# Optimization experiments

Hardware: AMD Instinct MI355X
Metric: run time of the kernel (lower is better)

## Reference

```python
import jax, jax.numpy as jnp
import numpy as np

H = 450    # hidden_size (JTNN default)
LAT = 56   # latent_size (tree_vec dim)
V = 780    # vocab size
T = 1024   # n_trees
L = 24     # nodes per tree (path topology)


def _tree_meta(Ln):
    # forward edge i: (i, i+1) eid=i ; reverse edge i: (i+1, i) eid=(Ln-1)+i
    n_f = Ln - 1
    eids, preds, srcs, dsts, labels = [], [], [], [], []
    for i in range(n_f):  # forward DFS steps
        eids.append(i); srcs.append(i); dsts.append(i + 1)
        preds.append(i - 1 if i > 0 else -1); labels.append(0)
    for k in range(n_f):  # backtrack DFS steps (reverse edges, deepest first)
        i = n_f - 1 - k
        eids.append(n_f + i); srcs.append(i + 1); dsts.append(i)
        preds.append(n_f + i + 1 if i < n_f - 1 else -1); labels.append(1)
    # incoming edges of the dst node v (for the node 'pull' h = sum of m)
    in1 = [d - 1 if d > 0 else -1 for d in dsts]
    in2 = [n_f + d if d < n_f else -1 for d in dsts]
    meta = [np.asarray(a, np.int32) for a in (eids, preds, srcs, dsts, in1, in2)]
    return meta, np.asarray(labels, np.float32)


def setup_inputs():
    key = jax.random.key(0)
    ks = jax.random.split(key, 12)
    s = 0.05
    return {
        "wid": jax.random.randint(ks[0], (T, L), 0, V, dtype=jnp.int32),
        "tree_vec": jax.random.normal(ks[1], (T, LAT), jnp.float32),
        "emb": jax.random.normal(ks[2], (V, H)) * s,
        "W_w": jax.random.normal(ks[3], (H + LAT, H)) * s, "W_b": jnp.zeros((H,)),
        "U_w": jax.random.normal(ks[4], (2 * H + LAT, H)) * s, "U_b": jnp.zeros((H,)),
        "Wo_w": jax.random.normal(ks[5], (H, V)) * s, "Wo_b": jnp.zeros((V,)),
        "Us_w": jax.random.normal(ks[6], (H, 1)) * s, "Us_b": jnp.zeros((1,)),
        "Wz_w": jax.random.normal(ks[7], (2 * H, H)) * s, "Wz_b": jnp.zeros((H,)),
        "Wr_w": jax.random.normal(ks[8], (H, H)) * s,
        "Ur_w": jax.random.normal(ks[9], (H, H)) * s, "Ur_b": jnp.zeros((H,)),
        "Wh_w": jax.random.normal(ks[10], (2 * H, H)) * s, "Wh_b": jnp.zeros((H,)),
    }


def reference(wid, tree_vec, emb, W_w, W_b, U_w, U_b, Wo_w, Wo_b, Us_w, Us_b,
              Wz_w, Wz_b, Wr_w, Ur_w, Ur_b, Wh_w, Wh_b):
    Tn, Ln = wid.shape
    n_f = Ln - 1
    nE = 2 * n_f
    meta, labels = _tree_meta(Ln)
    xs = tuple(jnp.asarray(a) for a in meta)
    x = emb[wid]                                  # [T, L, H] node features
    m0 = jnp.zeros((Tn, nE, H), x.dtype)
    rm0 = jnp.zeros((Tn, nE, H), x.dtype)

    def step(carry, sx_):
        m, rm = carry
        eid, pred, src, dst, i1, i2 = sx_
        gp = jnp.maximum(pred, 0)
        s = jnp.where(pred >= 0, m[:, gp], 0.0)        # line-graph pull: sum of m
        arm = jnp.where(pred >= 0, rm[:, gp], 0.0)     # accum_rm
        sxn = x[:, src]                                # src_x
        dxn = x[:, dst]                                # dst_x
        z = jax.nn.sigmoid(jnp.concatenate([sxn, s], 1) @ Wz_w + Wz_b)
        mt = jnp.tanh(jnp.concatenate([sxn, arm], 1) @ Wh_w + Wh_b)
        m_new = (1.0 - z) * s + z * mt
        r = jax.nn.sigmoid(dxn @ Wr_w + m_new @ Ur_w + Ur_b)
        m = m.at[:, eid].set(m_new)
        rm = rm.at[:, eid].set(r * m_new)
        # node pull on v: h_v = sum of m over incoming edges (post edge update)
        h_v = (jnp.where(i1 >= 0, m[:, jnp.maximum(i1, 0)], 0.0)
               + jnp.where(i2 >= 0, m[:, jnp.maximum(i2, 0)], 0.0))
        return (m, rm), (h_v, dxn)

    (_, _), (hs, xvs) = jax.lax.scan(step, (m0, rm0), xs)  # [nE, T, H] each

    tv_steps = jnp.broadcast_to(tree_vec, (nE, Tn, LAT))
    p_in = jnp.concatenate([
        jnp.concatenate([x[:, 0], jnp.zeros((Tn, H), x.dtype), tree_vec], 1),
        jnp.concatenate([xvs, hs, tv_steps], -1).reshape(-1, 2 * H + LAT),
    ], 0)
    q_in = jnp.concatenate([
        jnp.concatenate([jnp.zeros((Tn, H), x.dtype), tree_vec], 1),
        jnp.concatenate([hs[:n_f], tv_steps[:n_f]], -1).reshape(-1, H + LAT),
    ], 0)
    p_targets = jnp.concatenate([jnp.repeat(jnp.asarray(1.0 - labels), Tn),
                                 jnp.zeros((Tn,), jnp.float32)])
    q_targets = wid.T.reshape(-1)

    q_logits = jax.nn.relu(q_in @ W_w + W_b) @ Wo_w + Wo_b
    p_logit = (jax.nn.relu(p_in @ U_w + U_b) @ Us_w + Us_b)[:, 0]
    p_loss = jnp.sum(p_targets * jax.nn.softplus(-p_logit)
                     + (1.0 - p_targets) * jax.nn.softplus(p_logit)) / Tn
    logp = jax.nn.log_softmax(q_logits, -1)
    q_loss = -jnp.sum(jnp.take_along_axis(logp, q_targets[:, None], 1)) / Tn
    p_acc = jnp.mean(((p_logit > 0).astype(jnp.int32) == p_targets.astype(jnp.int32)).astype(jnp.float32))
    q_acc = jnp.mean((jnp.argmax(q_logits, 1) == q_targets).astype(jnp.float32))
    return (q_loss, p_loss, q_acc, p_acc)
```

## Files before the change

kernel.cpp:

```cpp
#include <hip/hip_runtime.h>
#include <hip/hip_bf16.h>
#include <math.h>

#define H 450
#define HP 464
#define KP 480
#define LAT 56
#define V 780
#define LW 24
#define NE 46
#define NF 23
#define SLOT (1024*HP)
#define SROWS 2048
#define QROWS (24*1024)
#define PROWS (47*1024)
#define PTGT  (23*1024)
#define QBLK 6144

typedef __hip_bfloat16 bf16;
typedef __attribute__((ext_vector_type(8))) short short8;
typedef __attribute__((ext_vector_type(4))) float f32x4;

#define MFMA16(a,b,c) __builtin_amdgcn_mfma_f32_16x16x32_bf16(a,b,c,0,0,0)

__device__ __forceinline__ float sigm(float x) { return 1.f / (1.f + expf(-x)); }
__device__ __forceinline__ float toF(bf16 x) { return __bfloat162float(x); }
__device__ __forceinline__ void stV(float* p, float v) { *p = v; }
__device__ __forceinline__ void stV(bf16* p, float v) { *p = __float2bfloat16(v); }
__device__ __forceinline__ short8 ld8(const bf16* p) { return *reinterpret_cast<const short8*>(p); }

__device__ __forceinline__ void gl_lds(const bf16* g, bf16* l) {
    __builtin_amdgcn_global_load_lds(
        (const __attribute__((address_space(1))) void*)g,
        (__attribute__((address_space(3))) void*)l, 16, 0, 0);
}

__device__ __forceinline__ void xcd_decode(int b, int C, int& row0, int& col0) {
    int rres = b & 7;
    int colt = (b >> 3) % C;
    int g    = b / (8 * C);
    row0 = (rres + 8 * g) * 64;
    col0 = colt * 64;
}
__device__ __forceinline__ void xcd_decode128(int b, int C, int& row0, int& col0) {
    int rres = b & 7;
    int colt = (b >> 3) % C;
    int g    = b / (8 * C);
    row0 = (rres + 8 * g) * 128;
    col0 = colt * 128;
}

__global__ __launch_bounds__(256)
void make_bt(const float* __restrict__ src, int K, int N, int ld,
             bf16* __restrict__ dst, int npad) {
    int idx = blockIdx.x * 256 + threadIdx.x;
    if (idx >= npad * KP) return;
    int n = idx / KP, k = idx - n * KP;
    float v = (n < N && k < K) ? src[(size_t)k * ld + n] : 0.f;
    dst[idx] = __float2bfloat16(v);
}

__global__ __launch_bounds__(256)
void zero_init(float* __restrict__ out, float* __restrict__ Sb, int n) {
    int i = blockIdx.x * 256 + threadIdx.x;
    if (i < 4) out[i] = 0.f;
    if (i < n) Sb[i] = 0.f;
}

__global__ __launch_bounds__(256)
void gather_x(const float* __restrict__ emb, const int* __restrict__ wid,
              bf16* __restrict__ x_all) {
    int e = blockIdx.x * 256 + threadIdx.x;
    if (e >= 24 * 1024 * 225) return;
    int row = e / 225, h2 = e - row * 225;
    int t = row >> 10, n = row & 1023;
    int v = wid[n * LW + t];
    float2 x = ((const float2*)(emb + (size_t)v * H))[h2];
    bf16* dst = x_all + (size_t)row * HP + 2 * h2;
    dst[0] = __float2bfloat16(x.x);
    dst[1] = __float2bfloat16(x.y);
}

template<typename TC>
__global__ __launch_bounds__(256)
void gemm128(const bf16* __restrict__ A, int lda,
             const bf16* __restrict__ Bt, int N, int cblk,
             TC* __restrict__ C, int ldc,
             const float* __restrict__ bias,
             const float* __restrict__ addrow, int addld, int relu) {
    __shared__ bf16 As[128 * 32];
    __shared__ bf16 Bs[128 * 32];
    int tid = threadIdx.x;
    int lane = tid & 63, wave = tid >> 6;
    int wx = wave & 1, wy = wave >> 1;
    int lrow = lane & 15, quad = lane >> 4;
    int row0, col0;
    xcd_decode128(blockIdx.x, cblk, row0, col0);
    f32x4 acc[4][4] = {};
    for (int k0i = 0; k0i < 15; k0i++) {
        int k0 = k0i * 32;
#pragma unroll
        for (int r = 0; r < 2; r++) {
            int t = r * 256 + tid;
            int row = t >> 2, ko = (t & 3) * 8;
            gl_lds(A  + (size_t)(row0 + row) * lda + k0 + ko, As + t * 8);
            gl_lds(Bt + (size_t)(col0 + row) * KP  + k0 + ko, Bs + t * 8);
        }
        __syncthreads();
        short8 a[4], b[4];
#pragma unroll
        for (int f = 0; f < 4; f++)
            a[f] = ld8(As + (wy * 64 + f * 16 + lrow) * 32 + quad * 8);
#pragma unroll
        for (int f = 0; f < 4; f++)
            b[f] = ld8(Bs + (wx * 64 + f * 16 + lrow) * 32 + quad * 8);
#pragma unroll
        for (int fi = 0; fi < 4; fi++)
#pragma unroll
            for (int fj = 0; fj < 4; fj++)
                acc[fi][fj] = MFMA16(a[fi], b[fj], acc[fi][fj]);
        __syncthreads();
    }
#pragma unroll
    for (int fi = 0; fi < 4; fi++)
#pragma unroll
        for (int e = 0; e < 4; e++) {
            int r = row0 + wy * 64 + fi * 16 + quad * 4 + e;
#pragma unroll
            for (int fj = 0; fj < 4; fj++) {
                int c = col0 + wx * 64 + fj * 16 + lrow;
                if (c >= N) continue;
                float v = acc[fi][fj][e];
                if (bias) v += bias[c];
                if (addrow) v += addrow[(size_t)(r & 1023) * addld + c];
                if (relu) v = fmaxf(v, 0.f);
                stV(&C[(size_t)r * ldc + c], v);
            }
        }
}

__global__ __launch_bounds__(256)
void p_gemm128(const bf16* __restrict__ hs, const bf16* __restrict__ UbT,
               const bf16* __restrict__ XUa, const float* __restrict__ Ptv,
               const float* __restrict__ Us, float* __restrict__ pl) {
    __shared__ bf16 As[128 * 32];
    __shared__ bf16 Bs[128 * 32];
    int tid = threadIdx.x;
    int lane = tid & 63, wave = tid >> 6;
    int wx = wave & 1, wy = wave >> 1;
    int lrow = lane & 15, quad = lane >> 4;
    int row0, col0;
    xcd_decode128(blockIdx.x, 4, row0, col0);
    f32x4 acc[4][4] = {};
    for (int k0i = 0; k0i < 15; k0i++) {
        int k0 = k0i * 32;
#pragma unroll
        for (int r = 0; r < 2; r++) {
            int t = r * 256 + tid;
            int row = t >> 2, ko = (t & 3) * 8;
            gl_lds(hs  + (size_t)(row0 + row) * HP + k0 + ko, As + t * 8);
            gl_lds(UbT + (size_t)(col0 + row) * KP + k0 + ko, Bs + t * 8);
        }
        __syncthreads();
        short8 a[4], b[4];
#pragma unroll
        for (int f = 0; f < 4; f++)
            a[f] = ld8(As + (wy * 64 + f * 16 + lrow) * 32 + quad * 8);
#pragma unroll
        for (int f = 0; f < 4; f++)
            b[f] = ld8(Bs + (wx * 64 + f * 16 + lrow) * 32 + quad * 8);
#pragma unroll
        for (int fi = 0; fi < 4; fi++)
#pragma unroll
            for (int fj = 0; fj < 4; fj++)
                acc[fi][fj] = MFMA16(a[fi], b[fj], acc[fi][fj]);
        __syncthreads();
    }
    int t0 = row0 >> 10;
#pragma unroll
    for (int fi = 0; fi < 4; fi++)
#pragma unroll
        for (int e = 0; e < 4; e++) {
            int r = row0 + wy * 64 + fi * 16 + quad * 4 + e;
            int t = r >> 10, n = r & 1023;
            int dst = (t < 23) ? (t + 1) : (45 - t);
            float part = 0.f;
#pragma unroll
            for (int fj = 0; fj < 4; fj++) {
                int c = col0 + wx * 64 + fj * 16 + lrow;
                if (c < H) {
                    float h = fmaxf(acc[fi][fj][e] + toF(XUa[((size_t)dst * 1024 + n) * H + c])
                                    + Ptv[(size_t)n * H + c], 0.f);
                    part += h * Us[c];
                }
            }
#pragma unroll
            for (int off = 1; off < 16; off <<= 1)
                part += __shfl_xor(part, off);
            if (lrow == 0) atomicAdd(&pl[1024 + r], part);
        }
    (void)t0;
}

__global__ __launch_bounds__(256)
void tv_gemm(const float* __restrict__ tv, const float* __restrict__ Wlat,
             const float* __restrict__ bias, float* __restrict__ out) {
    int n = blockIdx.y;
    int c = blockIdx.x * 256 + threadIdx.x;
    __shared__ float tvs[LAT];
    if (threadIdx.x < LAT) tvs[threadIdx.x] = tv[n * LAT + threadIdx.x];
    __syncthreads();
    if (c < H) {
        float a = bias[c];
#pragma unroll 8
        for (int k = 0; k < LAT; k++) a += tvs[k] * Wlat[(size_t)k * H + c];
        out[(size_t)n * H + c] = a;
    }
}

__global__ __launch_bounds__(256)
void scan_k1(const bf16* __restrict__ AsF, const bf16* __restrict__ AsB,
             const bf16* __restrict__ Arm,
             const bf16* __restrict__ BzT, const bf16* __restrict__ BhT,
             const bf16* __restrict__ Xz, const bf16* __restrict__ Xh,
             float* __restrict__ Sb, bf16* __restrict__ hsF, bf16* __restrict__ hsB,
             int u, int skip) {
    int tid = threadIdx.x;
    int lane = tid & 63, wave = tid >> 6;
    int wx = wave & 1, wy = wave >> 1;
    int lrow = lane & 15, quad = lane >> 4;
    int row0, col0;
    xcd_decode(blockIdx.x, 8, row0, col0);
    bool fwd = row0 < 1024;
    int rb = row0 & 1023;
    f32x4 az[2][2] = {}, ah[2][2] = {};
    if (!skip) {
        const bf16* As = (fwd ? AsF : AsB) + (size_t)(rb + wy * 32 + lrow) * HP + quad * 8;
        const bf16* Ar = Arm + (size_t)(row0 + wy * 32 + lrow) * HP + quad * 8;
        const bf16* bz0 = BzT + (size_t)(col0 + wx * 32 + lrow) * KP + quad * 8;
        const bf16* bh0 = BhT + (size_t)(col0 + wx * 32 + lrow) * KP + quad * 8;
        for (int k = 0; k < 15; k++) {
            short8 s0 = ld8(As + k * 32);
            short8 s1 = ld8(As + (size_t)16 * HP + k * 32);
            short8 r0 = ld8(Ar + k * 32);
            short8 r1 = ld8(Ar + (size_t)16 * HP + k * 32);
            short8 z0 = ld8(bz0 + k * 32);
            short8 z1 = ld8(bz0 + 16 * KP + k * 32);
            short8 h0 = ld8(bh0 + k * 32);
            short8 h1 = ld8(bh0 + 16 * KP + k * 32);
            az[0][0] = MFMA16(s0, z0, az[0][0]);
            az[0][1] = MFMA16(s0, z1, az[0][1]);
            az[1][0] = MFMA16(s1, z0, az[1][0]);
            az[1][1] = MFMA16(s1, z1, az[1][1]);
            ah[0][0] = MFMA16(r0, h0, ah[0][0]);
            ah[0][1] = MFMA16(r0, h1, ah[0][1]);
            ah[1][0] = MFMA16(r1, h0, ah[1][0]);
            ah[1][1] = MFMA16(r1, h1, ah[1][1]);
        }
    }
    int src = fwd ? u : 23 - u;
    bf16* hso = fwd ? hsF : hsB;
#pragma unroll
    for (int i = 0; i < 2; i++)
#pragma unroll
        for (int e = 0; e < 4; e++) {
            int r = row0 + wy * 32 + i * 16 + quad * 4 + e;
            int n = r & 1023;
#pragma unroll
            for (int j = 0; j < 2; j++) {
                int c = col0 + wx * 32 + j * 16 + lrow;
                if (c >= H) continue;
                float zp = az[i][j][e] + toF(Xz[((size_t)src * 1024 + n) * H + c]);
                float hp = ah[i][j][e] + toF(Xh[((size_t)src * 1024 + n) * H + c]);
                float s  = Sb[(size_t)r * H + c];
                float z  = sigm(zp);
                float mt = tanhf(hp);
                float mn = (1.f - z) * s + z * mt;
                Sb[(size_t)r * H + c] = mn;
                hso[(size_t)n * HP + c] = __float2bfloat16(mn);
            }
        }
}

__global__ __launch_bounds__(256)
void scan_k2(const bf16* __restrict__ AmF, const bf16* __restrict__ AmB,
             const bf16* __restrict__ UrT, const bf16* __restrict__ Xr,
             const float* __restrict__ Sb, bf16* __restrict__ RMb, int u) {
    int tid = threadIdx.x;
    int lane = tid & 63, wave = tid >> 6;
    int wx = wave & 1, wy = wave >> 1;
    int lrow = lane & 15, quad = lane >> 4;
    int row0, col0;
    xcd_decode(blockIdx.x, 8, row0, col0);
    bool fwd = row0 < 1024;
    int rb = row0 & 1023;
    const bf16* Am = (fwd ? AmF : AmB) + (size_t)(rb + wy * 32 + lrow) * HP + quad * 8;
    const bf16* b0 = UrT + (size_t)(col0 + wx * 32 + lrow) * KP + quad * 8;
    f32x4 acc[2][2] = {};
    for (int k = 0; k < 15; k++) {
        short8 a0 = ld8(Am + k * 32);
        short8 a1 = ld8(Am + (size_t)16 * HP + k * 32);
        short8 w0 = ld8(b0 + k * 32);
        short8 w1 = ld8(b0 + 16 * KP + k * 32);
        acc[0][0] = MFMA16(a0, w0, acc[0][0]);
        acc[0][1] = MFMA16(a0, w1, acc[0][1]);
        acc[1][0] = MFMA16(a1, w0, acc[1][0]);
        acc[1][1] = MFMA16(a1, w1, acc[1][1]);
    }
    int dst = fwd ? (u + 1) : (22 - u);
#pragma unroll
    for (int i = 0; i < 2; i++)
#pragma unroll
        for (int e = 0; e < 4; e++) {
            int r = row0 + wy * 32 + i * 16 + quad * 4 + e;
            int n = r & 1023;
#pragma unroll
            for (int j = 0; j < 2; j++) {
                int c = col0 + wx * 32 + j * 16 + lrow;
                if (c >= H) continue;
                float rp = acc[i][j][e] + toF(Xr[((size_t)dst * 1024 + n) * H + c]);
                float rr = sigm(rp);
                RMb[(size_t)r * HP + c] = __float2bfloat16(rr * Sb[(size_t)r * H + c]);
            }
        }
}

__global__ __launch_bounds__(256)
void hv_fixup(bf16* __restrict__ hs) {
    int idx = blockIdx.x * 256 + threadIdx.x;
    if (idx >= 22 * SLOT) return;
    int tl = idx / SLOT;
    int rem = idx - tl * SLOT;
    size_t a = (size_t)(23 + tl) * SLOT + rem;
    size_t b = (size_t)(21 - tl) * SLOT + rem;
    hs[a] = __float2bfloat16(toF(hs[a]) + toF(hs[b]));
}

__global__ __launch_bounds__(256)
void q_root(const float* __restrict__ Qtv, bf16* __restrict__ qh) {
    int idx = blockIdx.x * 256 + threadIdx.x;
    if (idx >= 1024 * H) return;
    int n = idx / H, c = idx - n * H;
    qh[(size_t)n * HP + c] = __float2bfloat16(fmaxf(Qtv[idx], 0.f));
}

__global__ __launch_bounds__(256)
void q_reduce(const float* __restrict__ ql, const int* __restrict__ wid,
              float* __restrict__ qred) {
    int wave = threadIdx.x >> 6, lane = threadIdx.x & 63;
    int r = blockIdx.x * 4 + wave;
    int t = r >> 10, n = r & 1023;
    int tgt = wid[n * LW + t];
    const float4* row4 = (const float4*)(ql + (size_t)r * V);
    float m = -3.4e38f, s = 0.f; int mi = 0x7fffffff;
#pragma unroll
    for (int k = 0; k < 4; k++) {
        int c4 = lane + 64 * k;
        if (c4 < 195) {
            float4 v4 = row4[c4];
            float vv[4] = {v4.x, v4.y, v4.z, v4.w};
#pragma unroll
            for (int e = 0; e < 4; e++) {
                float v = vv[e];
                if (v > m) { s = s * __expf(m - v) + 1.f; m = v; mi = c4 * 4 + e; }
                else s += __expf(v - m);
            }
        }
    }
#pragma unroll
    for (int off = 1; off < 64; off <<= 1) {
        float m2 = __shfl_xor(m, off);
        float s2 = __shfl_xor(s, off);
        int   i2 = __shfl_xor(mi, off);
        if (m2 > m || (m2 == m && i2 < mi)) {
            s = s2 + s * __expf(m - m2);
            m = m2; mi = i2;
        } else {
            s = s + s2 * __expf(m2 - m);
        }
    }
    __shared__ float lred[4][2];
    if (lane == 0) {
        float lse = m + logf(s);
        lred[wave][0] = lse - ql[(size_t)r * V + tgt];
        lred[wave][1] = (mi == tgt) ? 1.f : 0.f;
    }
    __syncthreads();
    if (threadIdx.x == 0) {
        qred[blockIdx.x * 2]     = lred[0][0] + lred[1][0] + lred[2][0] + lred[3][0];
        qred[blockIdx.x * 2 + 1] = lred[0][1] + lred[1][1] + lred[2][1] + lred[3][1];
    }
}

__global__ __launch_bounds__(256)
void q_final(const float* __restrict__ qred, float* __restrict__ out) {
    int tid = threadIdx.x;
    float L = 0.f, A = 0.f;
    for (int i = tid; i < QBLK; i += 256) { L += qred[2 * i]; A += qred[2 * i + 1]; }
    __shared__ float s1[256], s2[256];
    s1[tid] = L; s2[tid] = A;
    __syncthreads();
    for (int k = 128; k > 0; k >>= 1) {
        if (tid < k) { s1[tid] += s1[tid + k]; s2[tid] += s2[tid + k]; }
        __syncthreads();
    }
    if (tid == 0) {
        out[0] = s1[0] * (1.f / 1024.f);
        out[2] = s2[0] * (1.f / 24576.f);
    }
}

__global__ __launch_bounds__(256)
void p_init(float* __restrict__ pl, const float* __restrict__ Us_b) {
    int idx = blockIdx.x * 256 + threadIdx.x;
    if (idx < PROWS) pl[idx] = Us_b[0];
}

__global__ __launch_bounds__(256)
void p_root(const bf16* __restrict__ XUa, const float* __restrict__ Ptv,
            const float* __restrict__ Us, float* __restrict__ pl) {
    int n = blockIdx.x;
    int tid = threadIdx.x;
    const bf16* xa = XUa + (size_t)n * H;
    const float* pt = Ptv + (size_t)n * H;
    float s = 0.f;
    for (int c = tid; c < H; c += 256)
        s += fmaxf(toF(xa[c]) + pt[c], 0.f) * Us[c];
    __shared__ float red[256];
    red[tid] = s;
    __syncthreads();
    for (int k = 128; k > 0; k >>= 1) {
        if (tid < k) red[tid] += red[tid + k];
        __syncthreads();
    }
    if (tid == 0) atomicAdd(&pl[n], red[0]);
}

__global__ __launch_bounds__(256)
void p_final(const float* __restrict__ pl, float* __restrict__ out) {
    int r = blockIdx.x * 256 + threadIdx.x;
    int tid = threadIdx.x;
    float loss = 0.f, acc = 0.f;
    if (r < PROWS) {
        float l = pl[r];
        int tgt = (r < PTGT) ? 1 : 0;
        float x = tgt ? -l : l;
        loss = fmaxf(x, 0.f) + log1pf(expf(-fabsf(x)));
        int pred = (l > 0.f) ? 1 : 0;
        acc = (pred == tgt) ? 1.f : 0.f;
    }
    __shared__ float s1[256], s2[256];
    s1[tid] = loss; s2[tid] = acc;
    __syncthreads();
    for (int k = 128; k > 0; k >>= 1) {
        if (tid < k) { s1[tid] += s1[tid + k]; s2[tid] += s2[tid + k]; }
        __syncthreads();
    }
    if (tid == 0) {
        atomicAdd(&out[1], s1[0] * (1.f / 1024.f));
        atomicAdd(&out[3], s2[0] * (1.f / 48128.f));
    }
}

extern "C" void kernel_launch(void* const* d_in, const int* in_sizes, int n_in,
                              void* d_out, int out_size, void* d_ws, size_t ws_size,
                              hipStream_t stream) {
    const int*   wid  = (const int*)  d_in[0];
    const float* tv   = (const float*)d_in[1];
    const float* emb  = (const float*)d_in[2];
    const float* W_w  = (const float*)d_in[3];
    const float* W_b  = (const float*)d_in[4];
    const float* U_w  = (const float*)d_in[5];
    const float* U_b  = (const float*)d_in[6];
    const float* Wo_w = (const float*)d_in[7];
    const float* Wo_b = (const float*)d_in[8];
    const float* Us_w = (const float*)d_in[9];
    const float* Us_b = (const float*)d_in[10];
    const float* Wz_w = (const float*)d_in[11];
    const float* Wz_b = (const float*)d_in[12];
    const float* Wr_w = (const float*)d_in[13];
    const float* Ur_w = (const float*)d_in[14];
    const float* Ur_b = (const float*)d_in[15];
    const float* Wh_w = (const float*)d_in[16];
    const float* Wh_b = (const float*)d_in[17];
    float* out = (float*)d_out;

    char* base = (char*)d_ws;
    const size_t XBb = (size_t)QROWS * H * 2;
    bf16*  Xz   = (bf16*)(base);
    bf16*  Xh   = (bf16*)(base + XBb);
    bf16*  Xr   = (bf16*)(base + 2 * XBb);
    bf16*  XUa  = (bf16*)(base + 3 * XBb);
    bf16*  hs   = (bf16*)(base + 4 * XBb);
    bf16*  x_all = hs;
    char*  p1   = base + 4 * XBb + (size_t)NE * SLOT * 2;
    bf16*  RMb  = (bf16*)p1;                p1 += (size_t)SROWS * HP * 2;
    float* Sb   = (float*)p1;               p1 += (size_t)SROWS * H * 4;
    float* Qtv  = (float*)p1;               p1 += (size_t)1024 * H * 4;
    float* Ptv  = (float*)p1;               p1 += (size_t)1024 * H * 4;
    float* pl   = (float*)p1;               p1 += (size_t)PROWS * 4;
    float* qred = (float*)p1;               p1 += (size_t)QBLK * 2 * 4;
    bf16*  BT   = (bf16*)p1;
    const size_t BTS = (size_t)512 * KP;
    bf16 *WztT = BT,           *WhtT = BT + BTS,     *WrT = BT + 2*BTS,
         *UaT  = BT + 3*BTS,   *WzbT = BT + 4*BTS,   *WhbT = BT + 5*BTS,
         *UrT  = BT + 6*BTS,   *UbT  = BT + 7*BTS,   *WtopT = BT + 8*BTS,
         *WoT  = BT + 9*BTS;
    bf16*  qh = (bf16*)base;
    float* ql = (float*)(base + (size_t)QROWS * HP * 2);

    zero_init<<<(SROWS * H + 255) / 256, 256, 0, stream>>>(out, Sb, SROWS * H);
    int btg = (512 * KP + 255) / 256;
    make_bt<<<btg, 256, 0, stream>>>(Wz_w,            H, H, H, WztT, 512);
    make_bt<<<btg, 256, 0, stream>>>(Wh_w,            H, H, H, WhtT, 512);
    make_bt<<<btg, 256, 0, stream>>>(Wr_w,            H, H, H, WrT,  512);
    make_bt<<<btg, 256, 0, stream>>>(U_w,             H, H, H, UaT,  512);
    make_bt<<<btg, 256, 0, stream>>>(Wz_w + 450*450,  H, H, H, WzbT, 512);
    make_bt<<<btg, 256, 0, stream>>>(Wh_w + 450*450,  H, H, H, WhbT, 512);
    make_bt<<<btg, 256, 0, stream>>>(Ur_w,            H, H, H, UrT,  512);
    make_bt<<<btg, 256, 0, stream>>>(U_w + 450*450,   H, H, H, UbT,  512);
    make_bt<<<btg, 256, 0, stream>>>(W_w,             H, H, H, WtopT, 512);
    make_bt<<<(896 * KP + 255) / 256, 256, 0, stream>>>(Wo_w, H, V, V, WoT, 896);

    gather_x<<<(24 * 1024 * 225 + 255) / 256, 256, 0, stream>>>(emb, wid, x_all);
    int gPre = (QROWS / 128) * 4;
    gemm128<bf16><<<gPre, 256, 0, stream>>>(x_all, HP, WztT, H, 4, Xz,  H, Wz_b, (const float*)nullptr, H, 0);
    gemm128<bf16><<<gPre, 256, 0, stream>>>(x_all, HP, WhtT, H, 4, Xh,  H, Wh_b, (const float*)nullptr, H, 0);
    gemm128<bf16><<<gPre, 256, 0, stream>>>(x_all, HP, WrT,  H, 4, Xr,  H, Ur_b, (const float*)nullptr, H, 0);
    gemm128<bf16><<<gPre, 256, 0, stream>>>(x_all, HP, UaT,  H, 4, XUa, H, (const float*)nullptr, (const float*)nullptr, H, 0);

    tv_gemm<<<dim3(2, 1024), 256, 0, stream>>>(tv, W_w + 450*450, W_b, Qtv);
    tv_gemm<<<dim3(2, 1024), 256, 0, stream>>>(tv, U_w + 900*450, U_b, Ptv);

    for (int u = 0; u < 23; u++) {
        const bf16* AsF = hs + (size_t)(u - 1) * SLOT;
        const bf16* AsB = hs + (size_t)(22 + u) * SLOT;
        scan_k1<<<256, 256, 0, stream>>>(AsF, AsB, RMb, WzbT, WhbT, Xz, Xh,
                                         Sb, hs + (size_t)u * SLOT,
                                         hs + (size_t)(23 + u) * SLOT, u, u == 0 ? 1 : 0);
        if (u < 22)
            scan_k2<<<256, 256, 0, stream>>>(hs + (size_t)u * SLOT, hs + (size_t)(23 + u) * SLOT,
                                             UrT, Xr, Sb, RMb, u);
    }
    hv_fixup<<<(22 * SLOT + 255) / 256, 256, 0, stream>>>(hs);

    p_init<<<(PROWS + 255) / 256, 256, 0, stream>>>(pl, Us_b);
    p_root<<<1024, 256, 0, stream>>>(XUa, Ptv, Us_w, pl);
    p_gemm128<<<(PROWS - 1024) / 128 * 4, 256, 0, stream>>>(hs, UbT, XUa, Ptv, Us_w, pl);
    p_final<<<PROWS / 256, 256, 0, stream>>>(pl, out);

    q_root<<<(1024 * H + 255) / 256, 256, 0, stream>>>(Qtv, qh);
    gemm128<bf16><<<(NF * 1024 / 128) * 4, 256, 0, stream>>>(hs, HP, WtopT, H, 4,
                                                             qh + (size_t)1024 * HP, HP,
                                                             (const float*)nullptr, Qtv, H, 1);
    gemm128<float><<<(QROWS / 128) * 7, 256, 0, stream>>>(qh, HP, WoT, V, 7, ql, V,
                                                          Wo_b, (const float*)nullptr, H, 0);
    q_reduce<<<QBLK, 256, 0, stream>>>(ql, wid, qred);
    q_final<<<1, 256, 0, stream>>>(qred, out);

    (void)in_sizes; (void)n_in; (void)out_size; (void)ws_size;
}
```

Before: 1.197 ms.

## Fuse four input-projection GEMMs into one wide GEMM and swizzle LDS tiles

The four x_all projections (Wz, Wh, Wr/Ur bias, U top) become a single GEMM over a concatenated 1800-column weight matrix with a packed bias vector. The epilogue splits columns into the Xz/Xh/Xr/XUa buffers, which sit next to each other in the workspace. This cuts the column padding waste from 512 to 450 per matrix and reads the A tiles in one pass instead of four launches. Separately, all 128x128 GEMMs apply an XOR-style rotation to the k-chunk offset in LDS to reduce bank conflicts on the fragment reads.

Result: faster. 1.104 ms (-7.8%).

```diff
diff --git a/kernel.cpp b/kernel.cpp
--- a/kernel.cpp
+++ b/kernel.cpp
@@ -16,6 +16,7 @@
 #define PROWS (47*1024)
 #define PTGT  (23*1024)
 #define QBLK 6144
+#define XBSZ ((size_t)QROWS * H)
 
 typedef __hip_bfloat16 bf16;
 typedef __attribute__((ext_vector_type(8))) short short8;
@@ -58,6 +59,18 @@
     int n = idx / KP, k = idx - n * KP;
     float v = (n < N && k < K) ? src[(size_t)k * ld + n] : 0.f;
     dst[idx] = __float2bfloat16(v);
+}
+
+__global__ __launch_bounds__(256)
+void pack_bias(const float* __restrict__ zb, const float* __restrict__ hb,
+               const float* __restrict__ rb, float* __restrict__ bias4) {
+    int i = blockIdx.x * 256 + threadIdx.x;
+    if (i >= 1856) return;
+    float v = 0.f;
+    if (i < 450)       v = zb[i];
+    else if (i < 900)  v = hb[i - 450];
+    else if (i < 1350) v = rb[i - 900];
+    bias4[i] = v;
 }
 
 __global__ __launch_bounds__(256)
@@ -94,6 +107,7 @@
     int lane = tid & 63, wave = tid >> 6;
     int wx = wave & 1, wy = wave >> 1;
     int lrow = lane & 15, quad = lane >> 4;
+    int perm = ((quad + (lrow >> 1)) & 3) * 8;
     int row0, col0;
     xcd_decode128(blockIdx.x, cblk, row0, col0);
     f32x4 acc[4][4] = {};
@@ -101,19 +115,20 @@
         int k0 = k0i * 32;
 #pragma unroll
         for (int r = 0; r < 2; r++) {
-            int t = r * 256 + tid;
-            int row = t >> 2, ko = (t & 3) * 8;
-            gl_lds(A  + (size_t)(row0 + row) * lda + k0 + ko, As + t * 8);
-            gl_lds(Bt + (size_t)(col0 + row) * KP  + k0 + ko, Bs + t * 8);
+            int tt = r * 256 + tid;
+            int row = tt >> 2, cl = tt & 3;
+            int cg = (cl - (row >> 1)) & 3;
+            gl_lds(A  + (size_t)(row0 + row) * lda + k0 + cg * 8, As + tt * 8);
+            gl_lds(Bt + (size_t)(col0 + row) * KP  + k0 + cg * 8, Bs + tt * 8);
         }
         __syncthreads();
         short8 a[4], b[4];
 #pragma unroll
         for (int f = 0; f < 4; f++)
-            a[f] = ld8(As + (wy * 64 + f * 16 + lrow) * 32 + quad * 8);
+            a[f] = ld8(As + (wy * 64 + f * 16 + lrow) * 32 + perm);
 #pragma unroll
         for (int f = 0; f < 4; f++)
-            b[f] = ld8(Bs + (wx * 64 + f * 16 + lrow) * 32 + quad * 8);
+            b[f] = ld8(Bs + (wx * 64 + f * 16 + lrow) * 32 + perm);
 #pragma unroll
         for (int fi = 0; fi < 4; fi++)
 #pragma unroll
@@ -140,6 +155,63 @@
 }
 
 __global__ __launch_bounds__(256)
+void gemm128_pre(const bf16* __restrict__ A,
+                 const bf16* __restrict__ Bt,
+                 bf16* __restrict__ X0,
+                 const float* __restrict__ bias4) {
+    __shared__ bf16 As[128 * 32];
+    __shared__ bf16 Bs[128 * 32];
+    int tid = threadIdx.x;
+    int lane = tid & 63, wave = tid >> 6;
+    int wx = wave & 1, wy = wave >> 1;
+    int lrow = lane & 15, quad = lane >> 4;
+    int perm = ((quad + (lrow >> 1)) & 3) * 8;
+    int row0, col0;
+    xcd_decode128(blockIdx.x, 15, row0, col0);
+    f32x4 acc[4][4] = {};
+    for (int k0i = 0; k0i < 15; k0i++) {
+        int k0 = k0i * 32;
+#pragma unroll
+        for (int r = 0; r < 2; r++) {
+            int tt = r * 256 + tid;
+            int row = tt >> 2, cl = tt & 3;
+            int cg = (cl - (row >> 1)) & 3;
+            gl_lds(A  + (size_t)(row0 + row) * HP + k0 + cg * 8, As + tt * 8);
+            gl_lds(Bt + (size_t)(col0 + row) * KP + k0 + cg * 8, Bs + tt * 8);
+        }
+        __syncthreads();
+        short8 a[4], b[4];
+#pragma unroll
+        for (int f = 0; f < 4; f++)
+            a[f] = ld8(As + (wy * 64 + f * 16 + lrow) * 32 + perm);
+#pragma unroll
+        for (int f = 0; f < 4; f++)
+            b[f] = ld8(Bs + (wx * 64 + f * 16 + lrow) * 32 + perm);
+#pragma unroll
+        for (int fi = 0; fi < 4; fi++)
+#pragma unroll
+            for (int fj = 0; fj < 4; fj++)
+                acc[fi][fj] = MFMA16(a[fi], b[fj], acc[fi][fj]);
+        __syncthreads();
+    }
+#pragma unroll
+    for (int fi = 0; fi < 4; fi++)
+#pragma unroll
+        for (int e = 0; e < 4; e++) {
+            int r = row0 + wy * 64 + fi * 16 + quad * 4 + e;
+#pragma unroll
+            for (int fj = 0; fj < 4; fj++) {
+                int c = col0 + wx * 64 + fj * 16 + lrow;
+                if (c >= 1800) continue;
+                int mm = c / 450;
+                int cc = c - mm * 450;
+                float v = acc[fi][fj][e] + bias4[c];
+                X0[(size_t)mm * XBSZ + (size_t)r * H + cc] = __float2bfloat16(v);
+            }
+        }
+}
+
+__global__ __launch_bounds__(256)
 void p_gemm128(const bf16* __restrict__ hs, const bf16* __restrict__ UbT,
                const bf16* __restrict__ XUa, const float* __restrict__ Ptv,
                const float* __restrict__ Us, float* __restrict__ pl) {
@@ -149,6 +221,7 @@
     int lane = tid & 63, wave = tid >> 6;
     int wx = wave & 1, wy = wave >> 1;
     int lrow = lane & 15, quad = lane >> 4;
+    int perm = ((quad + (lrow >> 1)) & 3) * 8;
     int row0, col0;
     xcd_decode128(blockIdx.x, 4, row0, col0);
     f32x4 acc[4][4] = {};
@@ -156,19 +229,20 @@
         int k0 = k0i * 32;
 #pragma unroll
         for (int r = 0; r < 2; r++) {
-            int t = r * 256 + tid;
-            int row = t >> 2, ko = (t & 3) * 8;
-            gl_lds(hs  + (size_t)(row0 + row) * HP + k0 + ko, As + t * 8);
-            gl_lds(UbT + (size_t)(col0 + row) * KP + k0 + ko, Bs + t * 8);
+            int tt = r * 256 + tid;
+            int row = tt >> 2, cl = tt & 3;
+            int cg = (cl - (row >> 1)) & 3;
+            gl_lds(hs  + (size_t)(row0 + row) * HP + k0 + cg * 8, As + tt * 8);
+            gl_lds(UbT + (size_t)(col0 + row) * KP + k0 + cg * 8, Bs + tt * 8);
         }
         __syncthreads();
         short8 a[4], b[4];
 #pragma unroll
         for (int f = 0; f < 4; f++)
-            a[f] = ld8(As + (wy * 64 + f * 16 + lrow) * 32 + quad * 8);
+            a[f] = ld8(As + (wy * 64 + f * 16 + lrow) * 32 + perm);
 #pragma unroll
         for (int f = 0; f < 4; f++)
-            b[f] = ld8(Bs + (wx * 64 + f * 16 + lrow) * 32 + quad * 8);
+            b[f] = ld8(Bs + (wx * 64 + f * 16 + lrow) * 32 + perm);
 #pragma unroll
         for (int fi = 0; fi < 4; fi++)
 #pragma unroll
@@ -176,7 +250,6 @@
                 acc[fi][fj] = MFMA16(a[fi], b[fj], acc[fi][fj]);
         __syncthreads();
     }
-    int t0 = row0 >> 10;
 #pragma unroll
     for (int fi = 0; fi < 4; fi++)
 #pragma unroll
@@ -199,7 +272,6 @@
                 part += __shfl_xor(part, off);
             if (lrow == 0) atomicAdd(&pl[1024 + r], part);
         }
-    (void)t0;
 }
 
 __global__ __launch_bounds__(256)
@@ -486,7 +558,7 @@
     float* out = (float*)d_out;
 
     char* base = (char*)d_ws;
-    const size_t XBb = (size_t)QROWS * H * 2;
+    const size_t XBb = XBSZ * 2;
     bf16*  Xz   = (bf16*)(base);
     bf16*  Xh   = (bf16*)(base + XBb);
     bf16*  Xr   = (bf16*)(base + 2 * XBb);
@@ -500,21 +572,26 @@
     float* Ptv  = (float*)p1;               p1 += (size_t)1024 * H * 4;
     float* pl   = (float*)p1;               p1 += (size_t)PROWS * 4;
     float* qred = (float*)p1;               p1 += (size_t)QBLK * 2 * 4;
+    float* bias4 = (float*)p1;              p1 += (size_t)1856 * 4;
     bf16*  BT   = (bf16*)p1;
-    const size_t BTS = (size_t)512 * KP;
-    bf16 *WztT = BT,           *WhtT = BT + BTS,     *WrT = BT + 2*BTS,
-         *UaT  = BT + 3*BTS,   *WzbT = BT + 4*BTS,   *WhbT = BT + 5*BTS,
-         *UrT  = BT + 6*BTS,   *UbT  = BT + 7*BTS,   *WtopT = BT + 8*BTS,
-         *WoT  = BT + 9*BTS;
+    bf16* BT4   = BT;
+    bf16* WzbT  = BT + (size_t)1856 * KP;
+    bf16* WhbT  = WzbT + (size_t)512 * KP;
+    bf16* UrT   = WhbT + (size_t)512 * KP;
+    bf16* UbT   = UrT  + (size_t)512 * KP;
+    bf16* WtopT = UbT  + (size_t)512 * KP;
+    bf16* WoT   = WtopT + (size_t)512 * KP;
     bf16*  qh = (bf16*)base;
     float* ql = (float*)(base + (size_t)QROWS * HP * 2);
 
     zero_init<<<(SROWS * H + 255) / 256, 256, 0, stream>>>(out, Sb, SROWS * H);
     int btg = (512 * KP + 255) / 256;
-    make_bt<<<btg, 256, 0, stream>>>(Wz_w,            H, H, H, WztT, 512);
-    make_bt<<<btg, 256, 0, stream>>>(Wh_w,            H, H, H, WhtT, 512);
-    make_bt<<<btg, 256, 0, stream>>>(Wr_w,            H, H, H, WrT,  512);
-    make_bt<<<btg, 256, 0, stream>>>(U_w,             H, H, H, UaT,  512);
+    int btg450 = (450 * KP + 255) / 256;
+    make_bt<<<btg450, 256, 0, stream>>>(Wz_w, H, H, H, BT4,                        450);
+    make_bt<<<btg450, 256, 0, stream>>>(Wh_w, H, H, H, BT4 + (size_t)450 * KP,     450);
+    make_bt<<<btg450, 256, 0, stream>>>(Wr_w, H, H, H, BT4 + (size_t)900 * KP,     450);
+    make_bt<<<(506 * KP + 255) / 256, 256, 0, stream>>>(U_w, H, H, H, BT4 + (size_t)1350 * KP, 506);
+    pack_bias<<<8, 256, 0, stream>>>(Wz_b, Wh_b, Ur_b, bias4);
     make_bt<<<btg, 256, 0, stream>>>(Wz_w + 450*450,  H, H, H, WzbT, 512);
     make_bt<<<btg, 256, 0, stream>>>(Wh_w + 450*450,  H, H, H, WhbT, 512);
     make_bt<<<btg, 256, 0, stream>>>(Ur_w,            H, H, H, UrT,  512);
@@ -523,11 +600,7 @@
     make_bt<<<(896 * KP + 255) / 256, 256, 0, stream>>>(Wo_w, H, V, V, WoT, 896);
 
     gather_x<<<(24 * 1024 * 225 + 255) / 256, 256, 0, stream>>>(emb, wid, x_all);
-    int gPre = (QROWS / 128) * 4;
-    gemm128<bf16><<<gPre, 256, 0, stream>>>(x_all, HP, WztT, H, 4, Xz,  H, Wz_b, (const float*)nullptr, H, 0);
-    gemm128<bf16><<<gPre, 256, 0, stream>>>(x_all, HP, WhtT, H, 4, Xh,  H, Wh_b, (const float*)nullptr, H, 0);
-    gemm128<bf16><<<gPre, 256, 0, stream>>>(x_all, HP, WrT,  H, 4, Xr,  H, Ur_b, (const float*)nullptr, H, 0);
-    gemm128<bf16><<<gPre, 256, 0, stream>>>(x_all, HP, UaT,  H, 4, XUa, H, (const float*)nullptr, (const float*)nullptr, H, 0);
+    gemm128_pre<<<(QROWS / 128) * 15, 256, 0, stream>>>(x_all, BT4, Xz, bias4);
 
     tv_gemm<<<dim3(2, 1024), 256, 0, stream>>>(tv, W_w + 450*450, W_b, Qtv);
     tv_gemm<<<dim3(2, 1024), 256, 0, stream>>>(tv, U_w + 900*450, U_b, Ptv);
```
